# Optimization experiments

Hardware: AMD Instinct MI355X
Metric: run time of the kernel (lower is better)

Reference implementation:

```python
import jax, jax.numpy as jnp
import numpy as np

DIM = 2048
NUM_HEADS = 8
HEAD_DIM = DIM // NUM_HEADS  # 256; forward requires seq_len == HEAD_DIM
B = 64
N = HEAD_DIM  # q @ k (untransposed) only works when N == head_dim


def setup_inputs() -> dict:
    key = jax.random.key(0)
    k1, k2, k3, k4 = jax.random.split(key, 4)
    x = jax.random.normal(k1, (B, N, DIM), dtype=jnp.float32)
    # torch Linear stores weight as [out_features, in_features]
    w_qkv = jax.random.normal(k2, (3 * DIM, DIM), dtype=jnp.float32) * 0.02
    w_proj = jax.random.normal(k3, (DIM, DIM), dtype=jnp.float32) * 0.02
    b_proj = jax.random.normal(k4, (DIM,), dtype=jnp.float32) * 0.02
    return {"x": x, "w_qkv": w_qkv, "w_proj": w_proj, "b_proj": b_proj}


def reference(x, w_qkv, w_proj, b_proj):
    Bb, Nn, C = x.shape
    H, D = NUM_HEADS, C // NUM_HEADS
    # qkv projection (no bias), split into q,k,v of shape [B,H,N,D]
    qkv = (x @ w_qkv.T).reshape(Bb, Nn, 3, H, D).transpose(2, 0, 3, 1, 4)
    q, k, v = qkv[0], qkv[1], qkv[2]
    # NON-standard: q @ k with k NOT transposed -> contracts q's feature dim
    # against k's token dim (valid because D == N). attn: [B,H,N,N]
    attn = jnp.matmul(q, k)
    # transpose last two dims, then softmax over the new last axis
    attn = jnp.swapaxes(attn, -2, -1)
    attn = jax.nn.softmax(attn, axis=-1)
    out = jnp.matmul(attn, v)              # [B,H,N,D]
    out = out.swapaxes(1, 2).reshape(Bb, Nn, C)
    return out @ w_proj.T + b_proj
```

## Files before the change

kernel.cpp:

```cpp
#include <hip/hip_runtime.h>
#include <hip/hip_bf16.h>

typedef unsigned short u16;
typedef __attribute__((ext_vector_type(4))) float f32x4;
typedef __attribute__((ext_vector_type(8))) short short8;
typedef __attribute__((ext_vector_type(8))) u16 us8;


__device__ __forceinline__ u16 f2bf(float f) {
  union { float f; unsigned u; } v; v.f = f;
  unsigned r = v.u + 0x7fffu + ((v.u >> 16) & 1u);
  return (u16)(r >> 16);
}
__device__ __forceinline__ float bf2f(u16 h) {
  union { unsigned u; float f; } v; v.u = ((unsigned)h) << 16; return v.f;
}

__global__ void beacon_kernel(float* __restrict__ out, float val, int n) {
  int stride = gridDim.x * blockDim.x;
  for (int i = blockIdx.x * blockDim.x + threadIdx.x; i < n; i += stride)
    out[i] = val;
}

__global__ void split_kernel(const float* __restrict__ in, u16* __restrict__ hi,
                             u16* __restrict__ lo, int n4) {
  int stride = gridDim.x * blockDim.x;
  for (int i = blockIdx.x * blockDim.x + threadIdx.x; i < n4; i += stride) {
    f32x4 v = ((const f32x4*)in)[i];
    ushort4 h;
    h.x = f2bf(v[0]); h.y = f2bf(v[1]); h.z = f2bf(v[2]); h.w = f2bf(v[3]);
    ((ushort4*)hi)[i] = h;
    if (lo) {
      ushort4 l;
      l.x = f2bf(v[0] - bf2f(h.x)); l.y = f2bf(v[1] - bf2f(h.y));
      l.z = f2bf(v[2] - bf2f(h.z)); l.w = f2bf(v[3] - bf2f(h.w));
      ((ushort4*)lo)[i] = l;
    }
  }
}

#define SCHED0 __builtin_amdgcn_sched_barrier(0)
#define LGKM0 do { asm volatile("s_waitcnt lgkmcnt(0)" ::: "memory"); SCHED0; } while (0)
#define VM0 do { asm volatile("s_waitcnt vmcnt(0)" ::: "memory"); } while (0)
#define BAR __builtin_amdgcn_s_barrier()

template<int EPI>
__global__ __launch_bounds__(512, 2)
void gemm256(const u16* __restrict__ A0, const u16* __restrict__ A1,
             const u16* __restrict__ B0, const u16* __restrict__ B1,
             int ldA, int ldB, int ntiles, int segShift, int gridMx,
             u16* __restrict__ qh, u16* __restrict__ ql,
             u16* __restrict__ kh, u16* __restrict__ kl,
             u16* __restrict__ vv,
             float* __restrict__ fout, const float* __restrict__ bias) {
  extern __shared__ __align__(16) u16 lds[];

  const int tid = threadIdx.x;
  const int w = tid >> 6, lane = tid & 63;
  const int wr = w >> 2, wcn = w & 3;
  const int l15 = lane & 15, g = lane >> 4;
  const int rsw = l15 & 7;
  const int scol = (((tid & 7) ^ ((tid >> 3) & 7)) << 3);

  int bid = blockIdx.x, cpx = gridDim.x >> 3;
  int swz = (bid & 7) * cpx + (bid >> 3);
  int m0 = (swz % gridMx) << 8;
  int n0 = (swz / gridMx) << 8;

  const u16* As[2] = {A0, A1};
  const u16* Bs[2] = {B0, B1};
  const int kmask = (1 << segShift) - 1;

  f32x4 acc[8][4] = {};
  short8 af[8], bA[4], bB[4];

  auto stageA = [&](int db, const u16* Ab, int k0) {
    #pragma unroll
    for (int s = 0; s < 4; ++s) {
      const u16* src = Ab + (size_t)(m0 + s * 64 + (tid >> 3)) * ldA + k0 + scol;
      u16* dst = lds + db * 32768 + s * 4096 + tid * 8;
      __builtin_amdgcn_global_load_lds(
          (const __attribute__((address_space(1))) unsigned*)src,
          (__attribute__((address_space(3))) unsigned*)dst, 16, 0, 0);
    }
  };
  auto stageB = [&](int db, const u16* Bb, int k0) {
    #pragma unroll
    for (int s = 0; s < 4; ++s) {
      const u16* src = Bb + (size_t)(n0 + s * 64 + (tid >> 3)) * ldB + k0 + scol;
      u16* dst = lds + db * 32768 + 16384 + s * 4096 + tid * 8;
      __builtin_amdgcn_global_load_lds(
          (const __attribute__((address_space(1))) unsigned*)src,
          (__attribute__((address_space(3))) unsigned*)dst, 16, 0, 0);
    }
  };
  auto readA = [&](int db, int MH) {
    #pragma unroll
    for (int f = 0; f < 4; ++f) {
      int row = wr * 128 + MH * 64 + f * 16 + l15;
      #pragma unroll
      for (int kk = 0; kk < 2; ++kk) {
        int sl = (kk * 4 + g) ^ rsw;
        af[f * 2 + kk] = *(const short8*)(lds + db * 32768 + row * 64 + sl * 8);
      }
    }
  };
  auto readB = [&](short8* bf, int db, int NH) {
    #pragma unroll
    for (int f = 0; f < 2; ++f) {
      int row = wcn * 64 + NH * 32 + f * 16 + l15;
      #pragma unroll
      for (int kk = 0; kk < 2; ++kk) {
        int sl = (kk * 4 + g) ^ rsw;
        bf[f * 2 + kk] = *(const short8*)(lds + db * 32768 + 16384 + row * 64 + sl * 8);
      }
    }
  };

#define MMA_QUAD(MH, NH, BF)                                                   \
  __builtin_amdgcn_s_setprio(1);                                               \
  _Pragma("unroll") for (int f = 0; f < 4; ++f)                                \
    _Pragma("unroll") for (int j = 0; j < 2; ++j)                              \
      _Pragma("unroll") for (int kk = 0; kk < 2; ++kk)                         \
        acc[(MH) * 4 + f][(NH) * 2 + j] =                                      \
            __builtin_amdgcn_mfma_f32_16x16x32_bf16(                           \
                af[f * 2 + kk], BF[j * 2 + kk],                                \
                acc[(MH) * 4 + f][(NH) * 2 + j], 0, 0, 0);                     \
  __builtin_amdgcn_s_setprio(0)

  const int T = ntiles;
  stageA(0, As[0], 0);
  stageB(0, Bs[0], 0);
  VM0;
  BAR; SCHED0;

  for (int t = 0; t < T - 1; ++t) {
    int cur = t & 1, nxt = cur ^ 1;
    int t1 = t + 1;
    const u16* An = As[t1 >> segShift];
    const u16* Bn = Bs[t1 >> segShift];
    int kn = (t1 & kmask) << 6;
    readA(cur, 0);
    readB(bA, cur, 0);
    stageA(nxt, An, kn);
    BAR; LGKM0;
    MMA_QUAD(0, 0, bA);
    BAR; SCHED0;
    readB(bB, cur, 1);
    stageB(nxt, Bn, kn);
    BAR; LGKM0;
    MMA_QUAD(0, 1, bB);
    BAR; SCHED0;
    readA(cur, 1);
    BAR; LGKM0;
    MMA_QUAD(1, 1, bB);
    BAR; SCHED0;
    MMA_QUAD(1, 0, bA);
    VM0;
    BAR; SCHED0;
  }
  {
    int cur = (T - 1) & 1;
    readA(cur, 0);
    readB(bA, cur, 0);
    LGKM0;
    MMA_QUAD(0, 0, bA);
    readB(bB, cur, 1);
    LGKM0;
    MMA_QUAD(0, 1, bB);
    readA(cur, 1);
    LGKM0;
    MMA_QUAD(1, 1, bB);
    MMA_QUAD(1, 0, bA);
  }
#undef MMA_QUAD

  #pragma unroll
  for (int i = 0; i < 8; ++i)
    #pragma unroll
    for (int j = 0; j < 4; ++j)
      #pragma unroll
      for (int rr = 0; rr < 4; ++rr) {
        int gm = m0 + wr * 128 + i * 16 + g * 4 + rr;
        int gn = n0 + wcn * 64 + j * 16 + l15;
        float val = acc[i][j][rr];
        if constexpr (EPI == 0) {
          int b = gm >> 8, tok = gm & 255;
          int sel = gn >> 11, head = (gn >> 8) & 7, col = gn & 255;
          size_t addr = (((size_t)b * 8 + head) * 256 + tok) * 256 + col;
          u16 h = f2bf(val), lo = f2bf(val - bf2f(h));
          if (sel == 0) { qh[addr] = h; ql[addr] = lo; }
          else          { kh[addr] = h; kl[addr] = lo; }
        } else if constexpr (EPI == 1) {
          int b = gm >> 8, tok = gm & 255;
          int head = (gn >> 8) & 7, col = gn & 255;
          size_t addr = (((size_t)b * 8 + head) * 256 + tok) * 256 + col;
          vv[addr] = f2bf(val);
        } else {
          fout[(size_t)gm * 2048 + gn] = val + bias[gn];
        }
      }
}

__global__ __launch_bounds__(256)
void fused_attn(const u16* __restrict__ kh, const u16* __restrict__ kl,
                const u16* __restrict__ qh, const u16* __restrict__ ql,
                const u16* __restrict__ vT, u16* __restrict__ aout) {
  __shared__ __align__(16) u16 sA[2][2048];
  __shared__ __align__(16) u16 sB[2][8192];
  __shared__ __align__(16) u16 sP[64 * 276];
  __shared__ float red[2][4][64];

  const int tid = threadIdx.x;
  const int wave = tid >> 6, lane = tid & 63;
  const int l15 = lane & 15, l16 = lane >> 4;
  const int sxor = (l15 >> 1) & 3;
  const int scol = ((lane & 3) ^ ((lane >> 3) & 3)) * 8;

  const int bid = blockIdx.x;
  const int plane = (bid & 7) * 64 + (bid >> 5);
  const int mtile = (bid >> 3) & 3;
  const int m0 = mtile << 6;
  const size_t zo = (size_t)plane * 65536;
  const u16* As[3] = {kh + zo, kh + zo, kl + zo};
  const u16* Bs[3] = {qh + zo, ql + zo, qh + zo};

  auto stageL = [&](int db, int ks) {
    int seg = ks >> 3, k0 = (ks & 7) * 32;
    {
      const u16* gp = As[seg];
      int r = wave * 16 + (lane >> 2);
      const u16* src = gp + (size_t)(m0 + r) * 256 + k0 + scol;
      __builtin_amdgcn_global_load_lds(
          (const __attribute__((address_space(1))) unsigned*)src,
          (__attribute__((address_space(3))) unsigned*)(sA[db] + wave * 512), 16, 0, 0);
    }
    {
      const u16* gp = Bs[seg];
      #pragma unroll
      for (int c = 0; c < 4; ++c) {
        int chunk = wave + c * 4;
        int r = chunk * 16 + (lane >> 2);
        const u16* src = gp + (size_t)r * 256 + k0 + scol;
        __builtin_amdgcn_global_load_lds(
            (const __attribute__((address_space(1))) unsigned*)src,
            (__attribute__((address_space(3))) unsigned*)(sB[db] + chunk * 512), 16, 0, 0);
      }
    }
  };

  f32x4 acc[4][4] = {};
  stageL(0, 0);
  VM0; BAR; SCHED0;
  for (int ks = 0; ks < 24; ++ks) {
    int cur = ks & 1, nxt = cur ^ 1;
    short8 a[4], b[4];
    #pragma unroll
    for (int fi = 0; fi < 4; ++fi) {
      int ra = (fi * 16 + l15) * 4 + (l16 ^ sxor);
      a[fi] = ((const short8*)sA[cur])[ra];
    }
    #pragma unroll
    for (int fj = 0; fj < 4; ++fj) {
      int rb = ((wave * 64 + fj * 16 + l15)) * 4 + (l16 ^ sxor);
      b[fj] = ((const short8*)sB[cur])[rb];
    }
    if (ks < 23) stageL(nxt, ks + 1);
    BAR; LGKM0;
    #pragma unroll
    for (int fi = 0; fi < 4; ++fi)
      #pragma unroll
      for (int fj = 0; fj < 4; ++fj)
        acc[fi][fj] = __builtin_amdgcn_mfma_f32_16x16x32_bf16(a[fi], b[fj], acc[fi][fj], 0, 0, 0);
    if (ks < 23) VM0;
    BAR; SCHED0;
  }

  #pragma unroll
  for (int fi = 0; fi < 4; ++fi)
    #pragma unroll
    for (int rr = 0; rr < 4; ++rr) {
      float m = fmaxf(fmaxf(acc[fi][0][rr], acc[fi][1][rr]),
                      fmaxf(acc[fi][2][rr], acc[fi][3][rr]));
      #pragma unroll
      for (int sh = 1; sh < 16; sh <<= 1) m = fmaxf(m, __shfl_xor(m, sh));
      if (l15 == 0) red[0][wave][fi * 16 + l16 * 4 + rr] = m;
    }
  __syncthreads();
  #pragma unroll
  for (int fi = 0; fi < 4; ++fi)
    #pragma unroll
    for (int rr = 0; rr < 4; ++rr) {
      int i = fi * 16 + l16 * 4 + rr;
      float M = fmaxf(fmaxf(red[0][0][i], red[0][1][i]),
                      fmaxf(red[0][2][i], red[0][3][i]));
      float s = 0.f;
      #pragma unroll
      for (int fj = 0; fj < 4; ++fj) {
        float ev = __expf(acc[fi][fj][rr] - M);
        acc[fi][fj][rr] = ev;
        s += ev;
      }
      #pragma unroll
      for (int sh = 1; sh < 16; sh <<= 1) s += __shfl_xor(s, sh);
      if (l15 == 0) red[1][wave][i] = s;
    }
  __syncthreads();
  #pragma unroll
  for (int fi = 0; fi < 4; ++fi)
    #pragma unroll
    for (int rr = 0; rr < 4; ++rr) {
      int i = fi * 16 + l16 * 4 + rr;
      float S = (red[1][0][i] + red[1][1][i]) + (red[1][2][i] + red[1][3][i]);
      float inv = 1.0f / S;
      #pragma unroll
      for (int fj = 0; fj < 4; ++fj)
        sP[i * 276 + wave * 64 + fj * 16 + l15] = f2bf(acc[fi][fj][rr] * inv);
    }
  __syncthreads();

  const int wr2 = wave >> 1, wc2 = wave & 1;
  auto stageV = [&](int db, int ks) {
    int k0 = ks * 32;
    #pragma unroll
    for (int c = 0; c < 4; ++c) {
      int chunk = wave + c * 4;
      int r = chunk * 16 + (lane >> 2);
      const u16* src = vT + zo + (size_t)r * 256 + k0 + scol;
      __builtin_amdgcn_global_load_lds(
          (const __attribute__((address_space(1))) unsigned*)src,
          (__attribute__((address_space(3))) unsigned*)(sB[db] + chunk * 512), 16, 0, 0);
    }
  };
  f32x4 acc2[2][8] = {};
  stageV(0, 0);
  VM0; BAR; SCHED0;
  for (int ks = 0; ks < 8; ++ks) {
    int cur = ks & 1, nxt = cur ^ 1;
    int k0 = ks * 32;
    short8 a2[2], b2[8];
    #pragma unroll
    for (int i = 0; i < 2; ++i) {
      int prow = wr2 * 32 + i * 16 + l15;
      a2[i] = *(const short8*)(sP + prow * 276 + k0 + l16 * 8);
    }
    #pragma unroll
    for (int j = 0; j < 8; ++j) {
      int rb = (wc2 * 128 + j * 16 + l15) * 4 + (l16 ^ sxor);
      b2[j] = ((const short8*)sB[cur])[rb];
    }
    if (ks < 7) stageV(nxt, ks + 1);
    BAR; LGKM0;
    #pragma unroll
    for (int i = 0; i < 2; ++i)
      #pragma unroll
      for (int j = 0; j < 8; ++j)
        acc2[i][j] = __builtin_amdgcn_mfma_f32_16x16x32_bf16(a2[i], b2[j], acc2[i][j], 0, 0, 0);
    if (ks < 7) VM0;
    BAR; SCHED0;
  }

  #pragma unroll
  for (int i = 0; i < 2; ++i)
    #pragma unroll
    for (int j = 0; j < 8; ++j)
      #pragma unroll
      for (int rr = 0; rr < 4; ++rr) {
        int gi = m0 + wr2 * 32 + i * 16 + l16 * 4 + rr;
        int gd = wc2 * 128 + j * 16 + l15;
        size_t row = (size_t)(plane >> 3) * 256 + gi;
        size_t col = (size_t)(plane & 7) * 256 + gd;
        aout[row * 2048 + col] = f2bf(acc2[i][j][rr]);
      }
}

__global__ void transpose_inplace(u16* __restrict__ kh, u16* __restrict__ kl,
                                  u16* __restrict__ v) {
  __shared__ u16 ta[64][66], tb[64][66];
  u16* base = (blockIdx.z == 0) ? kh : (blockIdx.z == 1) ? kl : v;
  u16* pl = base + (size_t)blockIdx.y * 65536;
  const int RA[10] = {0,1,2,3, 0,0,0,1,1,2};
  const int CA[10] = {0,1,2,3, 1,2,3,2,3,3};
  int p = blockIdx.x;
  int R = RA[p], C = CA[p];
  bool diag = (R == C);
  int tid = threadIdx.x;
  int r = tid >> 2, c0 = (tid & 3) * 16;

  const us8* sa = (const us8*)(pl + (size_t)(R * 64 + r) * 256 + C * 64 + c0);
  us8 a0 = sa[0], a1 = sa[1];
  #pragma unroll
  for (int s = 0; s < 8; ++s) { ta[r][c0 + s] = a0[s]; ta[r][c0 + 8 + s] = a1[s]; }
  if (!diag) {
    const us8* sb = (const us8*)(pl + (size_t)(C * 64 + r) * 256 + R * 64 + c0);
    us8 b0 = sb[0], b1 = sb[1];
    #pragma unroll
    for (int s = 0; s < 8; ++s) { tb[r][c0 + s] = b0[s]; tb[r][c0 + 8 + s] = b1[s]; }
  }
  __syncthreads();
  us8 o0, o1;
  #pragma unroll
  for (int s = 0; s < 8; ++s) { o0[s] = ta[c0 + s][r]; o1[s] = ta[c0 + 8 + s][r]; }
  us8* da = (us8*)(pl + (size_t)(C * 64 + r) * 256 + R * 64 + c0);
  da[0] = o0; da[1] = o1;
  if (!diag) {
    us8 p0, p1;
    #pragma unroll
    for (int s = 0; s < 8; ++s) { p0[s] = tb[c0 + s][r]; p1[s] = tb[c0 + 8 + s][r]; }
    us8* db = (us8*)(pl + (size_t)(R * 64 + r) * 256 + C * 64 + c0);
    db[0] = p0; db[1] = p1;
  }
}

extern "C" void kernel_launch(void* const* d_in, const int* in_sizes, int n_in,
                              void* d_out, int out_size, void* d_ws, size_t ws_size,
                              hipStream_t stream) {
  const float* x  = (const float*)d_in[0];
  const float* wq = (const float*)d_in[1];
  const float* wp = (const float*)d_in[2];
  const float* bp = (const float*)d_in[3];
  float* out = (float*)d_out;
  char* ws = (char*)d_ws;

  const size_t MB = 1ull << 20;
  const size_t NEED = 432 * MB;
  if (ws_size < NEED) {
    beacon_kernel<<<2048, 256, 0, stream>>>(out, (float)(ws_size >> 20), 16384 * 2048);
    return;
  }

  u16* q_hi = (u16*)(ws);
  u16* q_lo = (u16*)(ws + 64 * MB);
  u16* k_hi = (u16*)(ws + 128 * MB);
  u16* k_lo = (u16*)(ws + 192 * MB);
  u16* vbuf = (u16*)(ws + 256 * MB);
  u16* x_hi = (u16*)(ws + 320 * MB);
  u16* w_hi = (u16*)(ws + 384 * MB);
  u16* w_lo = (u16*)(ws + 408 * MB);
  u16* attn = (u16*)(ws + 320 * MB);
  u16* wpb  = (u16*)(ws + 384 * MB);

  split_kernel<<<8192, 256, 0, stream>>>(x,  x_hi, nullptr, 16384 * 2048 / 4);
  split_kernel<<<4096, 256, 0, stream>>>(wq, w_hi, w_lo, 6144 * 2048 / 4);

  gemm256<0><<<1024, 512, 131072, stream>>>(
      x_hi, x_hi, w_hi, w_lo, 2048, 2048, 64, 5, 64,
      q_hi, q_lo, k_hi, k_lo, nullptr, nullptr, nullptr);
  const u16* wv = w_hi + (size_t)4096 * 2048;
  gemm256<1><<<512, 512, 131072, stream>>>(
      x_hi, x_hi, wv, wv, 2048, 2048, 32, 5, 64,
      nullptr, nullptr, nullptr, nullptr, vbuf, nullptr, nullptr);

  transpose_inplace<<<dim3(10, 512, 3), 256, 0, stream>>>(k_hi, k_lo, vbuf);

  fused_attn<<<2048, 256, 0, stream>>>(k_hi, k_lo, q_hi, q_lo, vbuf, attn);

  split_kernel<<<2048, 256, 0, stream>>>(wp, wpb, nullptr, 2048 * 2048 / 4);
  gemm256<2><<<512, 512, 131072, stream>>>(
      attn, attn, wpb, wpb, 2048, 2048, 32, 5, 64,
      nullptr, nullptr, nullptr, nullptr, nullptr, out, bp);
}
```

Baseline: 1.026 ms.

## Restructure GEMM main loop to one barrier per K tile

Replaces the four-phase main loop with one that loads all A and B fragments for the tile from LDS up front. It then issues the next tile's global-to-LDS staging and runs all 32 MFMAs in a single high-priority block, with one wait and barrier per iteration. The peeled last iteration is folded in through a `more` guard. This removes three of the four block-wide barriers per K tile. In exchange it gives up interleaving LDS reads with MFMA work and holds more fragment registers live, which may reduce occupancy.

```diff
diff --git a/kernel.cpp b/kernel.cpp
--- a/kernel.cpp
+++ b/kernel.cpp
@@ -72,7 +72,6 @@
   const int kmask = (1 << segShift) - 1;
 
   f32x4 acc[8][4] = {};
-  short8 af[8], bA[4], bB[4];
 
   auto stageA = [&](int db, const u16* Ab, int k0) {
     #pragma unroll
@@ -94,18 +93,18 @@
           (__attribute__((address_space(3))) unsigned*)dst, 16, 0, 0);
     }
   };
-  auto readA = [&](int db, int MH) {
+  auto readA2 = [&](short8* out8, int db, int MH) {
     #pragma unroll
     for (int f = 0; f < 4; ++f) {
       int row = wr * 128 + MH * 64 + f * 16 + l15;
       #pragma unroll
       for (int kk = 0; kk < 2; ++kk) {
         int sl = (kk * 4 + g) ^ rsw;
-        af[f * 2 + kk] = *(const short8*)(lds + db * 32768 + row * 64 + sl * 8);
-      }
-    }
-  };
-  auto readB = [&](short8* bf, int db, int NH) {
+        out8[f * 2 + kk] = *(const short8*)(lds + db * 32768 + row * 64 + sl * 8);
+      }
+    }
+  };
+  auto readB2 = [&](short8* bf, int db, int NH) {
     #pragma unroll
     for (int f = 0; f < 2; ++f) {
       int row = wcn * 64 + NH * 32 + f * 16 + l15;
@@ -117,16 +116,14 @@
     }
   };
 
-#define MMA_QUAD(MH, NH, BF)                                                   \
-  __builtin_amdgcn_s_setprio(1);                                               \
+#define MMA_QUAD(MH, NH, AF, BF)                                               \
   _Pragma("unroll") for (int f = 0; f < 4; ++f)                                \
     _Pragma("unroll") for (int j = 0; j < 2; ++j)                              \
       _Pragma("unroll") for (int kk = 0; kk < 2; ++kk)                         \
         acc[(MH) * 4 + f][(NH) * 2 + j] =                                      \
             __builtin_amdgcn_mfma_f32_16x16x32_bf16(                           \
-                af[f * 2 + kk], BF[j * 2 + kk],                                \
-                acc[(MH) * 4 + f][(NH) * 2 + j], 0, 0, 0);                     \
-  __builtin_amdgcn_s_setprio(0)
+                AF[f * 2 + kk], BF[j * 2 + kk],                                \
+                acc[(MH) * 4 + f][(NH) * 2 + j], 0, 0, 0);
 
   const int T = ntiles;
   stageA(0, As[0], 0);
@@ -134,44 +131,29 @@
   VM0;
   BAR; SCHED0;
 
-  for (int t = 0; t < T - 1; ++t) {
+  for (int t = 0; t < T; ++t) {
     int cur = t & 1, nxt = cur ^ 1;
-    int t1 = t + 1;
-    const u16* An = As[t1 >> segShift];
-    const u16* Bn = Bs[t1 >> segShift];
-    int kn = (t1 & kmask) << 6;
-    readA(cur, 0);
-    readB(bA, cur, 0);
-    stageA(nxt, An, kn);
-    BAR; LGKM0;
-    MMA_QUAD(0, 0, bA);
-    BAR; SCHED0;
-    readB(bB, cur, 1);
-    stageB(nxt, Bn, kn);
-    BAR; LGKM0;
-    MMA_QUAD(0, 1, bB);
-    BAR; SCHED0;
-    readA(cur, 1);
-    BAR; LGKM0;
-    MMA_QUAD(1, 1, bB);
-    BAR; SCHED0;
-    MMA_QUAD(1, 0, bA);
-    VM0;
-    BAR; SCHED0;
-  }
-  {
-    int cur = (T - 1) & 1;
-    readA(cur, 0);
-    readB(bA, cur, 0);
-    LGKM0;
-    MMA_QUAD(0, 0, bA);
-    readB(bB, cur, 1);
-    LGKM0;
-    MMA_QUAD(0, 1, bB);
-    readA(cur, 1);
-    LGKM0;
-    MMA_QUAD(1, 1, bB);
-    MMA_QUAD(1, 0, bA);
+    const bool more = (t + 1 < T);
+    short8 aF0[8], aF1[8], bF0[4], bF1[4];
+    readA2(aF0, cur, 0);
+    readB2(bF0, cur, 0);
+    readB2(bF1, cur, 1);
+    readA2(aF1, cur, 1);
+    if (more) {
+      int t1 = t + 1;
+      stageA(nxt, As[t1 >> segShift], (t1 & kmask) << 6);
+      stageB(nxt, Bs[t1 >> segShift], (t1 & kmask) << 6);
+    }
+    __builtin_amdgcn_s_setprio(1);
+    MMA_QUAD(0, 0, aF0, bF0);
+    MMA_QUAD(0, 1, aF0, bF1);
+    MMA_QUAD(1, 1, aF1, bF1);
+    MMA_QUAD(1, 0, aF1, bF0);
+    __builtin_amdgcn_s_setprio(0);
+    if (more) {
+      VM0;
+      BAR; SCHED0;
+    }
   }
 #undef MMA_QUAD
 
```

After: 1.018 ms. About the same (-0.8%).
